# Optimization experiments

Hardware: AMD Instinct MI355X
Metric: run time of the kernel (lower is better)

Reference implementation:

```python
import jax, jax.numpy as jnp
import numpy as np

BL = 512  # sliding-window block length (init arg bl)


def setup_inputs() -> dict:
    key = jax.random.key(0)
    ks = jax.random.split(key, 8)
    L, qd, vd, c = 65536, 64, 64, 32  # c = q_dim // r1 = 32
    w = lambda k, sh: jax.random.normal(k, sh, jnp.float32) * 0.05
    return {
        "x1": jax.random.normal(ks[0], (1, qd, L), jnp.float32),
        "x2": jnp.zeros((1, vd, L), jnp.float32),
        "mask": jnp.ones((1, 1, L), jnp.float32),
        "Wq": w(ks[1], (c, qd)), "bq": jnp.zeros((c,), jnp.float32),
        "Wk": w(ks[2], (c, qd)), "bk": jnp.zeros((c,), jnp.float32),
        "Wv": w(ks[3], (c, vd)), "bv": jnp.zeros((c,), jnp.float32),
        "Wo": w(ks[4], (vd, c)), "bo": jnp.zeros((vd,), jnp.float32),
    }


def _sliding_att(x1, mask, Wq, bq, Wk, bk, Wv, bv, Wo, bo):
    bl = BL
    half = bl // 2
    W = bl + 2 * half
    B, _, L = x1.shape  # B == 1 (asserted in original)
    c = Wq.shape[0]
    vd = Wo.shape[0]

    # 1x1 conv1d projections == per-timestep matmul
    q = jnp.einsum('oc,bcl->bol', Wq, x1) + bq[None, :, None]
    k = jnp.einsum('oc,bcl->bol', Wk, x1) + bk[None, :, None]
    v = jnp.einsum('oc,bcl->bol', Wv, x1) + bv[None, :, None]

    nb = -(-L // bl)
    padL = nb * bl - L
    if padL:
        q = jnp.pad(q, ((0, 0), (0, 0), (0, padL)))
        k = jnp.pad(k, ((0, 0), (0, 0), (0, padL)))
        v = jnp.pad(v, ((0, 0), (0, 0), (0, padL)))
    base = jnp.pad(mask[:, 0:1, :], ((0, 0), (0, 0), (0, padL)))  # (1,1,nb*bl)

    # per-block queries: (nb, c, bl)
    qb = q[0].reshape(c, nb, bl).transpose(1, 0, 2)

    # pad K/V/mask by half on each side, gather overlapping windows (nb, c, W)
    kp = jnp.pad(k, ((0, 0), (0, 0), (half, half)))[0]
    vp = jnp.pad(v, ((0, 0), (0, 0), (half, half)))[0]
    bp = jnp.pad(base, ((0, 0), (0, 0), (half, half)))[0, 0]
    idx = jnp.arange(nb)[:, None] * bl + jnp.arange(W)[None, :]  # (nb, W)
    kw = kp[:, idx].transpose(1, 0, 2)  # (nb, c, W)
    vw = vp[:, idx].transpose(1, 0, 2)  # (nb, c, W)
    bw = bp[idx]                        # (nb, W)

    # causal window mask: query i attends to left half + up to i inside block
    rows = jnp.arange(bl)[:, None]
    cols = jnp.arange(W)[None, :]
    wmask = (cols <= half + rows).astype(jnp.float32)  # (bl, W)
    fmask = wmask[None, :, :] * bw[:, None, :]          # (nb, bl, W)

    # scalar dot attention with log-mask softmax trick (as in original)
    energy = jnp.einsum('ncq,nck->nqk', qb, kw) / jnp.sqrt(jnp.float32(c))
    att = jax.nn.softmax(energy + jnp.log(fmask + 1e-9), axis=-1) * fmask
    out = jnp.einsum('nck,nqk->ncq', vw, att)  # (nb, c, bl)

    out = jax.nn.relu(out)
    out = jnp.einsum('oc,ncl->nol', Wo, out) + bo[None, :, None]  # (nb, vd, bl)
    out = out.transpose(1, 0, 2).reshape(1, vd, nb * bl)[:, :, :L]
    return out * mask[:, 0:1, :]


def reference(x1, x2, mask, Wq, bq, Wk, bk, Wv, bv, Wo, bo):
    # stage == 'encoder': x2 is unused (value projected from x1)
    return _sliding_att(x1, mask, Wq, bq, Wk, bk, Wv, bv, Wo, bo)
```

## Files before the change

kernel.cpp:

```cpp
#include <hip/hip_runtime.h>
#include <hip/hip_bf16.h>
#include <math.h>

#define C    32
#define QD   64
#define VD   64
#define BLK  512
#define HALF 256

typedef __attribute__((ext_vector_type(8))) short bf16x8;
typedef __attribute__((ext_vector_type(4))) float f32x4;

static __device__ inline unsigned short f2bf(float x) {
    union { float f; unsigned u; } v; v.f = x;
    unsigned r = v.u + 0x7FFFu + ((v.u >> 16) & 1u);
    return (unsigned short)(r >> 16);
}

static __device__ inline unsigned pk2(float a, float b) {
    union { __hip_bfloat162 h; unsigned u; } x;
    x.h = __float22bfloat162_rn(make_float2(a, b));
    return x.u;
}

__global__ __launch_bounds__(256, 4) void qkv_proj(
    const float* __restrict__ x1,
    const float* __restrict__ Wq, const float* __restrict__ bq,
    const float* __restrict__ Wk, const float* __restrict__ bk,
    const float* __restrict__ Wv, const float* __restrict__ bv,
    unsigned short* __restrict__ qT, unsigned short* __restrict__ kT,
    unsigned short* __restrict__ v2, int L)
{
    __shared__ uint4 lq[256], lk[256], lv[256];

    const int lane = threadIdx.x & 63;
    const int wv   = threadIdx.x >> 6;
    const int lo   = lane & 15;
    const int quad = lane >> 4;

    const int tile = blockIdx.x * 4 + wv;
    const int l    = tile * 16 + lo;
    const int ll   = wv * 16 + lo;

    float xv[16];
    #pragma unroll
    for (int kc = 0; kc < 2; ++kc)
        #pragma unroll
        for (int j = 0; j < 8; ++j)
            xv[kc * 8 + j] = x1[(size_t)(kc * 32 + quad * 8 + j) * L + l];

    bf16x8 B[2];
    #pragma unroll
    for (int kc = 0; kc < 2; ++kc) {
        union { unsigned u[4]; bf16x8 v; } bb;
        #pragma unroll
        for (int p = 0; p < 4; ++p)
            bb.u[p] = pk2(xv[kc * 8 + 2 * p], xv[kc * 8 + 2 * p + 1]);
        B[kc] = bb.v;
    }

    const f32x4 zero = {0.f, 0.f, 0.f, 0.f};
    f32x4 acc[3][2];
    #pragma unroll
    for (int kind = 0; kind < 3; ++kind) {
        const float* __restrict__ Wp = (kind == 0) ? Wq : ((kind == 1) ? Wk : Wv);
        const float sc = (kind == 0) ? 0.17677669529663689f : 1.0f;
        #pragma unroll
        for (int ot = 0; ot < 2; ++ot) {
            f32x4 a = zero;
            #pragma unroll
            for (int kc = 0; kc < 2; ++kc) {
                const float* wp = Wp + (size_t)(ot * 16 + lo) * QD + kc * 32 + quad * 8;
                const float4 w0 = *(const float4*)wp;
                const float4 w1 = *(const float4*)(wp + 4);
                union { unsigned u[4]; bf16x8 v; } t;
                t.u[0] = pk2(w0.x * sc, w0.y * sc);
                t.u[1] = pk2(w0.z * sc, w0.w * sc);
                t.u[2] = pk2(w1.x * sc, w1.y * sc);
                t.u[3] = pk2(w1.z * sc, w1.w * sc);
                a = __builtin_amdgcn_mfma_f32_16x16x32_bf16(t.v, B[kc], a, 0, 0, 0);
            }
            acc[kind][ot] = a;
        }
    }

    #pragma unroll
    for (int kind = 0; kind < 2; ++kind) {
        const float* __restrict__ bp = (kind == 0) ? bq : bk;
        const float sc = (kind == 0) ? 0.17677669529663689f : 1.0f;
        unsigned* __restrict__ ld = (unsigned*)((kind == 0) ? lq : lk);
        #pragma unroll
        for (int ot = 0; ot < 2; ++ot) {
            const float4 b4 = *(const float4*)(bp + ot * 16 + quad * 4);
            const float r0 = acc[kind][ot][0] + b4.x * sc;
            const float r1 = acc[kind][ot][1] + b4.y * sc;
            const float r2 = acc[kind][ot][2] + b4.z * sc;
            const float r3 = acc[kind][ot][3] + b4.w * sc;
            ld[ll * 16 + ot * 8 + quad * 2 + 0] = pk2(r0, r1);
            ld[ll * 16 + ot * 8 + quad * 2 + 1] = pk2(r2, r3);
        }
    }
    {
        unsigned short* __restrict__ lvs = (unsigned short*)lv;
        const int vb = ((ll >> 5) << 10) + (ll & 31);
        #pragma unroll
        for (int ot = 0; ot < 2; ++ot) {
            const float4 b4 = *(const float4*)(bv + ot * 16 + quad * 4);
            const float* bp4 = (const float*)&b4;
            #pragma unroll
            for (int r = 0; r < 4; ++r)
                lvs[vb + (ot * 16 + quad * 4 + r) * 32] = f2bf(acc[2][ot][r] + bp4[r]);
        }
    }

    __syncthreads();

    const int t = threadIdx.x;
    const size_t blk16 = (size_t)blockIdx.x * 256;
    ((uint4*)qT)[blk16 + t] = lq[t];
    ((uint4*)kT)[blk16 + t] = lk[t];
    ((uint4*)v2)[blk16 + t] = lv[t];
}

__global__ __launch_bounds__(256, 4) void att_kernel(
    const unsigned short* __restrict__ qT,
    const unsigned short* __restrict__ kT,
    const unsigned short* __restrict__ v2,
    const float* __restrict__ mask,
    const float* __restrict__ Wo, const float* __restrict__ bo,
    float* __restrict__ out, int L)
{
    __shared__ unsigned short sK[2][2048];
    __shared__ unsigned short sV[2][2048];

    const int tid  = threadIdx.x;
    const int lane = tid & 63;
    const int wv   = tid >> 6;
    const int lo   = lane & 15;
    const int quad = lane >> 4;

    const int id  = blockIdx.x;
    const int w   = id & 127;
    const int sub = 7 - (id >> 7);
    const int s   = sub * 4 + wv;
    const int wq0 = w * BLK + s * 16;

    const int kstart = max(0, w * BLK - HALF);
    const int nwv  = ((wq0 + 15 - kstart) >> 6) + 1;
    const int nmax = ((w * BLK + (sub * 4 + 3) * 16 + 15 - kstart) >> 6) + 1;
    const int myq  = wq0 + lo;

    const bf16x8 qB = *(const bf16x8*)(qT + (size_t)myq * C + quad * 8);

    const f32x4 zero = {0.f, 0.f, 0.f, 0.f};
    f32x4 O0 = zero, O1 = zero;
    float psum = 0.f;

    const int qsl = lo + 16 * ((quad & 1) << 1);

    const int wrOff = (tid * 16) ^ (((tid >> 3) & 3) << 4);
    const int rdX   = (quad << 4) ^ (((lo >> 1) & 3) << 4);

    {
        const uint4 gk = ((const uint4*)(kT + (size_t)kstart * C))[tid];
        const uint4 gv = ((const uint4*)(v2 + ((size_t)(kstart >> 6) << 11)))[tid];
        *(uint4*)((char*)sK[0] + wrOff) = gk;
        *(uint4*)((char*)sV[0] + wrOff) = gv;
    }
    __syncthreads();

    for (int j = 0; j < nmax; ++j) {
        const int kb  = kstart + (j << 6);
        const int cur = j & 1;
        const bool more = (j + 1) < nmax;

        uint4 gk, gv;
        if (more) {
            const int kb1 = kb + 64;
            gk = ((const uint4*)(kT + (size_t)kb1 * C))[tid];
            gv = ((const uint4*)(v2 + ((size_t)(kb1 >> 6) << 11)))[tid];
        }

        if (j < nwv) {
            f32x4 S[4];
            float4 fm4[4];
            const char* kbuf = (const char*)sK[cur];
            #pragma unroll
            for (int t = 0; t < 4; ++t) {
                const bf16x8 kA = *(const bf16x8*)(kbuf + ((t * 16 + lo) * 64 + rdX));
                S[t] = __builtin_amdgcn_mfma_f32_16x16x32_bf16(kA, qB, zero, 0, 0, 0);
                fm4[t] = *(const float4*)(mask + kb + t * 16 + quad * 4);
            }

            unsigned wp[4][2];
            if (j == nwv - 1) {
                #pragma unroll
                for (int t = 0; t < 4; ++t) {
                    const float* fmp = (const float*)&fm4[t];
                    float p[4];
                    #pragma unroll
                    for (int r = 0; r < 4; ++r) {
                        const int key = kb + t * 16 + quad * 4 + r;
                        const float pd = (key <= myq) ? __expf(S[t][r]) * (fmp[r] + 1e-9f) : 0.f;
                        psum += pd;
                        p[r] = pd * fmp[r];
                    }
                    wp[t][0] = pk2(p[0], p[1]);
                    wp[t][1] = pk2(p[2], p[3]);
                }
            } else {
                #pragma unroll
                for (int t = 0; t < 4; ++t) {
                    const float* fmp = (const float*)&fm4[t];
                    float p[4];
                    #pragma unroll
                    for (int r = 0; r < 4; ++r) {
                        const float pd = __expf(S[t][r]) * (fmp[r] + 1e-9f);
                        psum += pd;
                        p[r] = pd * fmp[r];
                    }
                    wp[t][0] = pk2(p[0], p[1]);
                    wp[t][1] = pk2(p[2], p[3]);
                }
            }

            const char* vbuf = (const char*)sV[cur];
            #pragma unroll
            for (int g = 0; g < 2; ++g) {
                union { int i[4]; bf16x8 v; } pb;
                #pragma unroll
                for (int i = 0; i < 4; ++i) {
                    const int src = qsl + 16 * (i >> 1);
                    const int v0 = __shfl((int)wp[2 * g][i & 1], src);
                    const int v1 = __shfl((int)wp[2 * g + 1][i & 1], src);
                    pb.i[i] = (quad < 2) ? v0 : v1;
                }
                const bf16x8 vA0 = *(const bf16x8*)(vbuf + (g * 2048 + lo * 64 + rdX));
                const bf16x8 vA1 = *(const bf16x8*)(vbuf + (g * 2048 + (16 + lo) * 64 + rdX));
                O0 = __builtin_amdgcn_mfma_f32_16x16x32_bf16(vA0, pb.v, O0, 0, 0, 0);
                O1 = __builtin_amdgcn_mfma_f32_16x16x32_bf16(vA1, pb.v, O1, 0, 0, 0);
            }
        }

        if (more) {
            *(uint4*)((char*)sK[cur ^ 1] + wrOff) = gk;
            *(uint4*)((char*)sV[cur ^ 1] + wrOff) = gv;
        }
        __syncthreads();
    }

    float dsum = psum;
    dsum += __shfl_xor(dsum, 16);
    dsum += __shfl_xor(dsum, 32);
    const float inv = 1.f / dsum;

    unsigned tw[2][2];
    tw[0][0] = pk2(fmaxf(O0[0] * inv, 0.f), fmaxf(O0[1] * inv, 0.f));
    tw[0][1] = pk2(fmaxf(O0[2] * inv, 0.f), fmaxf(O0[3] * inv, 0.f));
    tw[1][0] = pk2(fmaxf(O1[0] * inv, 0.f), fmaxf(O1[1] * inv, 0.f));
    tw[1][1] = pk2(fmaxf(O1[2] * inv, 0.f), fmaxf(O1[3] * inv, 0.f));

    union { int i[4]; bf16x8 v; } tb;
    #pragma unroll
    for (int i = 0; i < 4; ++i) {
        const int src = qsl + 16 * (i >> 1);
        const int v0 = __shfl((int)tw[0][i & 1], src);
        const int v1 = __shfl((int)tw[1][i & 1], src);
        tb.i[i] = (quad < 2) ? v0 : v1;
    }

    const float mk = mask[myq];
    #pragma unroll
    for (int t = 0; t < 4; ++t) {
        float wtmp[8];
        *(float4*)&wtmp[0] = *(const float4*)(Wo + (size_t)(t * 16 + lo) * C + quad * 8);
        *(float4*)&wtmp[4] = *(const float4*)(Wo + (size_t)(t * 16 + lo) * C + quad * 8 + 4);
        union { unsigned u[4]; bf16x8 v; } wo;
        #pragma unroll
        for (int i = 0; i < 4; ++i) wo.u[i] = pk2(wtmp[2 * i], wtmp[2 * i + 1]);
        const f32x4 R = __builtin_amdgcn_mfma_f32_16x16x32_bf16(wo.v, tb.v, zero, 0, 0, 0);
        const float4 bo4 = *(const float4*)(bo + t * 16 + quad * 4);
        const float* bop = (const float*)&bo4;
        #pragma unroll
        for (int r = 0; r < 4; ++r)
            out[(size_t)(t * 16 + quad * 4 + r) * L + myq] = (R[r] + bop[r]) * mk;
    }
}

extern "C" void kernel_launch(void* const* d_in, const int* in_sizes, int n_in,
                              void* d_out, int out_size, void* d_ws, size_t ws_size,
                              hipStream_t stream)
{
    const float* x1   = (const float*)d_in[0];
    const float* mask = (const float*)d_in[2];
    const float* Wq   = (const float*)d_in[3];
    const float* bq   = (const float*)d_in[4];
    const float* Wk   = (const float*)d_in[5];
    const float* bk   = (const float*)d_in[6];
    const float* Wv   = (const float*)d_in[7];
    const float* bv   = (const float*)d_in[8];
    const float* Wo   = (const float*)d_in[9];
    const float* bo   = (const float*)d_in[10];
    float* out = (float*)d_out;

    const int L = in_sizes[0] / QD;
    unsigned short* qT = (unsigned short*)d_ws;
    unsigned short* kT = qT + (size_t)L * C;
    unsigned short* v2 = kT + (size_t)L * C;

    hipLaunchKernelGGL(qkv_proj, dim3(L / 64), dim3(256), 0, stream,
                       x1, Wq, bq, Wk, bk, Wv, bv, qT, kT, v2, L);

    hipLaunchKernelGGL(att_kernel, dim3(L / 64), dim3(256), 0, stream,
                       qT, kT, v2, mask, Wo, bo, out, L);
}
```

Baseline: 126.5 us.

## Fuse QKV projection into attention kernel, recomputing K/V per window tile

Merges the separate QKV projection kernel into the attention kernel. Each block now projects its own queries into shared memory and recomputes K and V for each 64-key tile from x1 while the previous tile is being consumed. This drops the workspace round trip and one kernel launch. In exchange, K/V projection work is repeated across overlapping windows and sub-blocks, raw fp32 x1 is read several times, and more registers are held for the resident weight fragments.

After: 195.2 us. 1.54x slower.

```diff
diff --git a/kernel.cpp b/kernel.cpp
--- a/kernel.cpp
+++ b/kernel.cpp
@@ -23,54 +23,140 @@
     return x.u;
 }
 
-__global__ __launch_bounds__(256, 4) void qkv_proj(
+static __device__ __attribute__((always_inline)) void proj_stage(
+    const float (&xv)[16], const bf16x8 (&WA)[2][2][2],
+    const float* __restrict__ bk, const float* __restrict__ bv,
+    unsigned short* __restrict__ kbuf, unsigned short* __restrict__ vbuf,
+    const int ll2, const int quad)
+{
+    bf16x8 Bx[2];
+    #pragma unroll
+    for (int kc = 0; kc < 2; ++kc) {
+        union { unsigned u[4]; bf16x8 v; } bb;
+        #pragma unroll
+        for (int p = 0; p < 4; ++p)
+            bb.u[p] = pk2(xv[kc * 8 + 2 * p], xv[kc * 8 + 2 * p + 1]);
+        Bx[kc] = bb.v;
+    }
+    const f32x4 zero = {0.f, 0.f, 0.f, 0.f};
+    f32x4 ak[2], av[2];
+    #pragma unroll
+    for (int ot = 0; ot < 2; ++ot) {
+        f32x4 a = zero, b = zero;
+        #pragma unroll
+        for (int kc = 0; kc < 2; ++kc) {
+            a = __builtin_amdgcn_mfma_f32_16x16x32_bf16(WA[0][ot][kc], Bx[kc], a, 0, 0, 0);
+            b = __builtin_amdgcn_mfma_f32_16x16x32_bf16(WA[1][ot][kc], Bx[kc], b, 0, 0, 0);
+        }
+        ak[ot] = a; av[ot] = b;
+    }
+    {
+        uint2* kd2 = (uint2*)kbuf;
+        const int sw = ((ll2 >> 1) & 3) << 2;
+        #pragma unroll
+        for (int ot = 0; ot < 2; ++ot) {
+            const float4 b4 = *(const float4*)(bk + ot * 16 + quad * 4);
+            uint2 d;
+            d.x = pk2(ak[ot][0] + b4.x, ak[ot][1] + b4.y);
+            d.y = pk2(ak[ot][2] + b4.z, ak[ot][3] + b4.w);
+            const int di = ll2 * 16 + ot * 8 + quad * 2;
+            kd2[(di ^ sw) >> 1] = d;
+        }
+    }
+    {
+        const int g = ll2 >> 5, k2 = ll2 & 31;
+        #pragma unroll
+        for (int ot = 0; ot < 2; ++ot) {
+            const float4 b4 = *(const float4*)(bv + ot * 16 + quad * 4);
+            const float* bp4 = (const float*)&b4;
+            #pragma unroll
+            for (int r = 0; r < 4; ++r) {
+                const int ch = ot * 16 + quad * 4 + r;
+                vbuf[g * 1024 + ch * 32 + (k2 ^ (((ch >> 1) & 3) << 3))] =
+                    f2bf(av[ot][r] + bp4[r]);
+            }
+        }
+    }
+}
+
+__global__ __launch_bounds__(256, 4) void fused_att(
     const float* __restrict__ x1,
+    const float* __restrict__ mask,
     const float* __restrict__ Wq, const float* __restrict__ bq,
     const float* __restrict__ Wk, const float* __restrict__ bk,
     const float* __restrict__ Wv, const float* __restrict__ bv,
-    unsigned short* __restrict__ qT, unsigned short* __restrict__ kT,
-    unsigned short* __restrict__ v2, int L)
+    const float* __restrict__ Wo, const float* __restrict__ bo,
+    float* __restrict__ out, int L)
 {
-    __shared__ uint4 lq[256], lk[256], lv[256];
-
-    const int lane = threadIdx.x & 63;
-    const int wv   = threadIdx.x >> 6;
+    __shared__ unsigned short sK[2][2048];
+    __shared__ unsigned short sV[2][2048];
+    __shared__ unsigned short sQ[2048];
+
+    const int tid  = threadIdx.x;
+    const int lane = tid & 63;
+    const int wvi  = tid >> 6;
     const int lo   = lane & 15;
     const int quad = lane >> 4;
 
-    const int tile = blockIdx.x * 4 + wv;
-    const int l    = tile * 16 + lo;
-    const int ll   = wv * 16 + lo;
-
-    float xv[16];
-    #pragma unroll
-    for (int kc = 0; kc < 2; ++kc)
-        #pragma unroll
-        for (int j = 0; j < 8; ++j)
-            xv[kc * 8 + j] = x1[(size_t)(kc * 32 + quad * 8 + j) * L + l];
-
-    bf16x8 B[2];
-    #pragma unroll
-    for (int kc = 0; kc < 2; ++kc) {
-        union { unsigned u[4]; bf16x8 v; } bb;
-        #pragma unroll
-        for (int p = 0; p < 4; ++p)
-            bb.u[p] = pk2(xv[kc * 8 + 2 * p], xv[kc * 8 + 2 * p + 1]);
-        B[kc] = bb.v;
-    }
+    const int id  = blockIdx.x;
+    const int w   = id & 127;
+    const int sub = 7 - (id >> 7);
+    const int s   = sub * 4 + wvi;
+    const int wq0 = w * BLK + s * 16;
+
+    const int kstart = max(0, w * BLK - HALF);
+    const int nwv  = ((wq0 + 15 - kstart) >> 6) + 1;
+    const int nmax = ((w * BLK + (sub * 4 + 3) * 16 + 15 - kstart) >> 6) + 1;
+    const int myq  = wq0 + lo;
+    const int ll2  = wvi * 16 + lo;
 
     const f32x4 zero = {0.f, 0.f, 0.f, 0.f};
-    f32x4 acc[3][2];
-    #pragma unroll
-    for (int kind = 0; kind < 3; ++kind) {
-        const float* __restrict__ Wp = (kind == 0) ? Wq : ((kind == 1) ? Wk : Wv);
-        const float sc = (kind == 0) ? 0.17677669529663689f : 1.0f;
+
+    bf16x8 WA[2][2][2];
+    #pragma unroll
+    for (int kind = 0; kind < 2; ++kind) {
+        const float* __restrict__ Wp = kind ? Wv : Wk;
+        #pragma unroll
+        for (int ot = 0; ot < 2; ++ot) {
+            #pragma unroll
+            for (int kc = 0; kc < 2; ++kc) {
+                const float* wp = Wp + (size_t)(ot * 16 + lo) * QD + kc * 32 + quad * 8;
+                const float4 w0 = *(const float4*)wp;
+                const float4 w1 = *(const float4*)(wp + 4);
+                union { unsigned u[4]; bf16x8 v; } t;
+                t.u[0] = pk2(w0.x, w0.y);
+                t.u[1] = pk2(w0.z, w0.w);
+                t.u[2] = pk2(w1.x, w1.y);
+                t.u[3] = pk2(w1.z, w1.w);
+                WA[kind][ot][kc] = t.v;
+            }
+        }
+    }
+
+    {
+        float xq[16];
+        #pragma unroll
+        for (int kc = 0; kc < 2; ++kc)
+            #pragma unroll
+            for (int jj = 0; jj < 8; ++jj)
+                xq[kc * 8 + jj] = x1[(size_t)(kc * 32 + quad * 8 + jj) * L + myq];
+        bf16x8 Bq[2];
+        #pragma unroll
+        for (int kc = 0; kc < 2; ++kc) {
+            union { unsigned u[4]; bf16x8 v; } bb;
+            #pragma unroll
+            for (int p = 0; p < 4; ++p)
+                bb.u[p] = pk2(xq[kc * 8 + 2 * p], xq[kc * 8 + 2 * p + 1]);
+            Bq[kc] = bb.v;
+        }
+        const float sc = 0.17677669529663689f;
+        unsigned* qd = (unsigned*)sQ;
         #pragma unroll
         for (int ot = 0; ot < 2; ++ot) {
             f32x4 a = zero;
             #pragma unroll
             for (int kc = 0; kc < 2; ++kc) {
-                const float* wp = Wp + (size_t)(ot * 16 + lo) * QD + kc * 32 + quad * 8;
+                const float* wp = Wq + (size_t)(ot * 16 + lo) * QD + kc * 32 + quad * 8;
                 const float4 w0 = *(const float4*)wp;
                 const float4 w1 = *(const float4*)(wp + 4);
                 union { unsigned u[4]; bf16x8 v; } t;
@@ -78,107 +164,47 @@
                 t.u[1] = pk2(w0.z * sc, w0.w * sc);
                 t.u[2] = pk2(w1.x * sc, w1.y * sc);
                 t.u[3] = pk2(w1.z * sc, w1.w * sc);
-                a = __builtin_amdgcn_mfma_f32_16x16x32_bf16(t.v, B[kc], a, 0, 0, 0);
-            }
-            acc[kind][ot] = a;
-        }
-    }
-
-    #pragma unroll
-    for (int kind = 0; kind < 2; ++kind) {
-        const float* __restrict__ bp = (kind == 0) ? bq : bk;
-        const float sc = (kind == 0) ? 0.17677669529663689f : 1.0f;
-        unsigned* __restrict__ ld = (unsigned*)((kind == 0) ? lq : lk);
-        #pragma unroll
-        for (int ot = 0; ot < 2; ++ot) {
-            const float4 b4 = *(const float4*)(bp + ot * 16 + quad * 4);
-            const float r0 = acc[kind][ot][0] + b4.x * sc;
-            const float r1 = acc[kind][ot][1] + b4.y * sc;
-            const float r2 = acc[kind][ot][2] + b4.z * sc;
-            const float r3 = acc[kind][ot][3] + b4.w * sc;
-            ld[ll * 16 + ot * 8 + quad * 2 + 0] = pk2(r0, r1);
-            ld[ll * 16 + ot * 8 + quad * 2 + 1] = pk2(r2, r3);
-        }
-    }
+                a = __builtin_amdgcn_mfma_f32_16x16x32_bf16(t.v, Bq[kc], a, 0, 0, 0);
+            }
+            const float4 b4 = *(const float4*)(bq + ot * 16 + quad * 4);
+            qd[ll2 * 16 + ot * 8 + quad * 2 + 0] = pk2(a[0] + b4.x * sc, a[1] + b4.y * sc);
+            qd[ll2 * 16 + ot * 8 + quad * 2 + 1] = pk2(a[2] + b4.z * sc, a[3] + b4.w * sc);
+        }
+    }
+
     {
-        unsigned short* __restrict__ lvs = (unsigned short*)lv;
-        const int vb = ((ll >> 5) << 10) + (ll & 31);
-        #pragma unroll
-        for (int ot = 0; ot < 2; ++ot) {
-            const float4 b4 = *(const float4*)(bv + ot * 16 + quad * 4);
-            const float* bp4 = (const float*)&b4;
-            #pragma unroll
-            for (int r = 0; r < 4; ++r)
-                lvs[vb + (ot * 16 + quad * 4 + r) * 32] = f2bf(acc[2][ot][r] + bp4[r]);
-        }
-    }
-
+        float x0[16];
+        const int l0 = kstart + ll2;
+        #pragma unroll
+        for (int kc = 0; kc < 2; ++kc)
+            #pragma unroll
+            for (int jj = 0; jj < 8; ++jj)
+                x0[kc * 8 + jj] = x1[(size_t)(kc * 32 + quad * 8 + jj) * L + l0];
+        proj_stage(x0, WA, bk, bv, sK[0], sV[0], ll2, quad);
+    }
     __syncthreads();
 
-    const int t = threadIdx.x;
-    const size_t blk16 = (size_t)blockIdx.x * 256;
-    ((uint4*)qT)[blk16 + t] = lq[t];
-    ((uint4*)kT)[blk16 + t] = lk[t];
-    ((uint4*)v2)[blk16 + t] = lv[t];
-}
-
-__global__ __launch_bounds__(256, 4) void att_kernel(
-    const unsigned short* __restrict__ qT,
-    const unsigned short* __restrict__ kT,
-    const unsigned short* __restrict__ v2,
-    const float* __restrict__ mask,
-    const float* __restrict__ Wo, const float* __restrict__ bo,
-    float* __restrict__ out, int L)
-{
-    __shared__ unsigned short sK[2][2048];
-    __shared__ unsigned short sV[2][2048];
-
-    const int tid  = threadIdx.x;
-    const int lane = tid & 63;
-    const int wv   = tid >> 6;
-    const int lo   = lane & 15;
-    const int quad = lane >> 4;
-
-    const int id  = blockIdx.x;
-    const int w   = id & 127;
-    const int sub = 7 - (id >> 7);
-    const int s   = sub * 4 + wv;
-    const int wq0 = w * BLK + s * 16;
-
-    const int kstart = max(0, w * BLK - HALF);
-    const int nwv  = ((wq0 + 15 - kstart) >> 6) + 1;
-    const int nmax = ((w * BLK + (sub * 4 + 3) * 16 + 15 - kstart) >> 6) + 1;
-    const int myq  = wq0 + lo;
-
-    const bf16x8 qB = *(const bf16x8*)(qT + (size_t)myq * C + quad * 8);
-
-    const f32x4 zero = {0.f, 0.f, 0.f, 0.f};
+    const bf16x8 qB = *(const bf16x8*)((const char*)sQ + ll2 * 64 + quad * 16);
+
     f32x4 O0 = zero, O1 = zero;
     float psum = 0.f;
 
     const int qsl = lo + 16 * ((quad & 1) << 1);
-
-    const int wrOff = (tid * 16) ^ (((tid >> 3) & 3) << 4);
-    const int rdX   = (quad << 4) ^ (((lo >> 1) & 3) << 4);
-
-    {
-        const uint4 gk = ((const uint4*)(kT + (size_t)kstart * C))[tid];
-        const uint4 gv = ((const uint4*)(v2 + ((size_t)(kstart >> 6) << 11)))[tid];
-        *(uint4*)((char*)sK[0] + wrOff) = gk;
-        *(uint4*)((char*)sV[0] + wrOff) = gv;
-    }
-    __syncthreads();
+    const int rdX = (quad << 4) ^ (((lo >> 1) & 3) << 4);
 
     for (int j = 0; j < nmax; ++j) {
         const int kb  = kstart + (j << 6);
         const int cur = j & 1;
         const bool more = (j + 1) < nmax;
 
-        uint4 gk, gv;
+        float xn[16];
         if (more) {
-            const int kb1 = kb + 64;
-            gk = ((const uint4*)(kT + (size_t)kb1 * C))[tid];
-            gv = ((const uint4*)(v2 + ((size_t)(kb1 >> 6) << 11)))[tid];
+            const int ln = kb + 64 + ll2;
+            #pragma unroll
+            for (int kc = 0; kc < 2; ++kc)
+                #pragma unroll
+                for (int jj = 0; jj < 8; ++jj)
+                    xn[kc * 8 + jj] = x1[(size_t)(kc * 32 + quad * 8 + jj) * L + ln];
         }
 
         if (j < nwv) {
@@ -242,10 +268,8 @@
             }
         }
 
-        if (more) {
-            *(uint4*)((char*)sK[cur ^ 1] + wrOff) = gk;
-            *(uint4*)((char*)sV[cur ^ 1] + wrOff) = gv;
-        }
+        if (more)
+            proj_stage(xn, WA, bk, bv, sK[cur ^ 1], sV[cur ^ 1], ll2, quad);
         __syncthreads();
     }
 
@@ -304,13 +328,8 @@
     float* out = (float*)d_out;
 
     const int L = in_sizes[0] / QD;
-    unsigned short* qT = (unsigned short*)d_ws;
-    unsigned short* kT = qT + (size_t)L * C;
-    unsigned short* v2 = kT + (size_t)L * C;
-
-    hipLaunchKernelGGL(qkv_proj, dim3(L / 64), dim3(256), 0, stream,
-                       x1, Wq, bq, Wk, bk, Wv, bv, qT, kT, v2, L);
-
-    hipLaunchKernelGGL(att_kernel, dim3(L / 64), dim3(256), 0, stream,
-                       qT, kT, v2, mask, Wo, bo, out, L);
-}
+    (void)d_ws; (void)ws_size;
+
+    hipLaunchKernelGGL(fused_att, dim3(L / 64), dim3(256), 0, stream,
+                       x1, mask, Wq, bq, Wk, bk, Wv, bv, Wo, bo, out, L);
+}
```
